# Kernel tuning notes

Measured on AMD Instinct MI355X. Metric: run time of the kernel, lower is better.

## Reference

```python
import jax, jax.numpy as jnp
import numpy as np

B, S, D_IN = 2, 2048, 2048
H, G, HD = 16, 4, 128          # num_heads, num_kv_groups, head_dim
GROUP = H // G                  # 4 query heads per kv group
D_OUT = H * HD                  # 2048
EPS = 1e-6


def _rope_tables(seq_len, head_dim, theta=10000.0):
    inv = 1.0 / (theta ** (np.arange(0, head_dim, 2, dtype=np.float32) / head_dim))
    pos = np.arange(seq_len, dtype=np.float32)
    ang = np.outer(pos, inv)                      # [S, HD/2]
    ang = np.concatenate([ang, ang], axis=-1)     # [S, HD]
    return jnp.asarray(np.cos(ang)), jnp.asarray(np.sin(ang))


def setup_inputs() -> dict:
    key = jax.random.key(0)
    ks = jax.random.split(key, 6)
    x = jax.random.normal(ks[0], (B, S, D_IN), dtype=jnp.float32)
    # Linear weights stored as [in, out] so y = x @ W (same math as nn.Linear)
    Wq = jax.random.normal(ks[1], (D_IN, 2 * D_OUT), dtype=jnp.float32) * (D_IN ** -0.5)
    Wk = jax.random.normal(ks[2], (D_IN, G * HD), dtype=jnp.float32) * (D_IN ** -0.5)
    Wv = jax.random.normal(ks[3], (D_IN, G * HD), dtype=jnp.float32) * (D_IN ** -0.5)
    Wo = jax.random.normal(ks[4], (D_OUT, D_IN), dtype=jnp.float32) * (D_OUT ** -0.5)
    q_norm_w = jnp.zeros((HD,), dtype=jnp.float32)  # Qwen-style zero-init (scale = 1 + w)
    k_norm_w = jnp.zeros((HD,), dtype=jnp.float32)
    cos, sin = _rope_tables(S, HD)
    mask = jnp.triu(jnp.ones((S, S), dtype=bool), k=1)  # causal: True above diagonal is masked
    return {"x": x, "Wq": Wq, "Wk": Wk, "Wv": Wv, "Wo": Wo,
            "q_norm_w": q_norm_w, "k_norm_w": k_norm_w,
            "cos": cos, "sin": sin, "mask": mask}


def _rmsnorm(x, w):
    xf = x.astype(jnp.float32)
    n = xf * jax.lax.rsqrt(jnp.mean(xf * xf, axis=-1, keepdims=True) + EPS)
    return (n * (1.0 + w.astype(jnp.float32))).astype(x.dtype)


def _apply_rope(x, cos, sin):
    # x: [..., S, HD]; full-dim rotation (rot_dim == head_dim)
    s = x.shape[-2]
    c = cos[:s][None, None]
    sn = sin[:s][None, None]
    x1, x2 = x[..., : HD // 2], x[..., HD // 2 :]
    rotated = jnp.concatenate([-x2, x1], axis=-1)
    return (x * c + rotated * sn).astype(x.dtype)


def reference(x, Wq, Wk, Wv, Wo, q_norm_w, k_norm_w, cos, sin, mask):
    b, s, _ = x.shape
    qg = (x @ Wq).reshape(b, s, H, 2 * HD)
    q, gate = qg[..., :HD], qg[..., HD:]
    gate = gate.reshape(b, s, D_OUT)
    q = q.transpose(0, 2, 1, 3)                                 # [b,H,s,HD]
    k = (x @ Wk).reshape(b, s, G, HD).transpose(0, 2, 1, 3)     # [b,G,s,HD]
    v = (x @ Wv).reshape(b, s, G, HD).transpose(0, 2, 1, 3)
    q = _rmsnorm(q, q_norm_w)
    k = _rmsnorm(k, k_norm_w)
    q = _apply_rope(q, cos, sin)
    k = _apply_rope(k, cos, sin)
    # GQA: group query heads by kv group instead of repeat_interleave on k/v
    qg4 = q.reshape(b, G, GROUP, s, HD)
    scores = jnp.einsum("bgjqd,bgkd->bgjqk", qg4, k)            # [b,G,GROUP,s,s]
    scores = jnp.where(mask[None, None, None], -jnp.inf, scores)
    w = jax.nn.softmax((scores * (HD ** -0.5)).astype(jnp.float32), axis=-1).astype(q.dtype)
    ctx = jnp.einsum("bgjqk,bgkd->bgjqd", w, v)                 # [b,G,GROUP,s,HD]
    ctx = ctx.reshape(b, H, s, HD).transpose(0, 2, 1, 3).reshape(b, s, D_OUT)
    ctx = ctx * jax.nn.sigmoid(gate)
    return ctx @ Wo
```

## Files before the change

### kernel.cpp

```cpp
#include <hip/hip_runtime.h>

#define S_LEN 2048
#define NROWS 4096
#define DIN   2048
#define DQKV  5120
#define DQG   4096

typedef __bf16 bf16x8 __attribute__((ext_vector_type(8)));
typedef float  floatx4 __attribute__((ext_vector_type(4)));
typedef unsigned short u16;

#define QK_SCALE 0.08838834764831845f

__device__ __forceinline__ u16 f2bf(float f) {
  unsigned int u = __float_as_uint(f);
  u += 0x7fffu + ((u >> 16) & 1u);
  return (u16)(u >> 16);
}
__device__ __forceinline__ float bf2f(u16 v) {
  return __uint_as_float(((unsigned int)v) << 16);
}
__device__ __forceinline__ int swz(int col, int row) {
  return (col & ~63) | ((((col >> 3) & 7) ^ (row & 7)) << 3) | (col & 7);
}

__device__ __forceinline__ void gload_lds16(const void* g, void* l) {
  __builtin_amdgcn_global_load_lds(
      (__attribute__((address_space(1))) void*)(void*)(g),
      (__attribute__((address_space(3))) void*)(l), 16, 0, 0);
}

__global__ __launch_bounds__(256) void cvt_x(const float* __restrict__ src,
                                             u16* __restrict__ dst) {
  const int i = blockIdx.x * 256 + threadIdx.x;
  const int row = i >> 9, col = (i & 511) << 2;
  const float4 v = reinterpret_cast<const float4*>(src)[i];
  ushort4 o;
  o.x = f2bf(v.x); o.y = f2bf(v.y); o.z = f2bf(v.z); o.w = f2bf(v.w);
  *reinterpret_cast<ushort4*>(dst + (size_t)row * DIN + swz(col, row)) = o;
}

__global__ __launch_bounds__(256) void tcvt(const float* __restrict__ src,
                                            u16* __restrict__ dst,
                                            int R, int C, int dld) {
  __shared__ float tile[32][33];
  const int c0 = blockIdx.x * 32, r0 = blockIdx.y * 32;
  const int t = threadIdx.x;
  {
    const int rl = t >> 3, cl4 = (t & 7) * 4;
    const float4 v = *reinterpret_cast<const float4*>(src + (size_t)(r0 + rl) * C + c0 + cl4);
    tile[rl][cl4 + 0] = v.x; tile[rl][cl4 + 1] = v.y;
    tile[rl][cl4 + 2] = v.z; tile[rl][cl4 + 3] = v.w;
  }
  __syncthreads();
  {
    const int cl = t >> 3, rl4 = (t & 7) * 4;
    ushort4 o;
    o.x = f2bf(tile[rl4 + 0][cl]); o.y = f2bf(tile[rl4 + 1][cl]);
    o.z = f2bf(tile[rl4 + 2][cl]); o.w = f2bf(tile[rl4 + 3][cl]);
    const int rd = c0 + cl, cd = r0 + rl4;
    *reinterpret_cast<ushort4*>(dst + (size_t)rd * dld + swz(cd, rd)) = o;
  }
}

template <bool BF16_OUT>
__global__ __launch_bounds__(256) void gemm_bt(const u16* __restrict__ A,
                                               const u16* __restrict__ Bt,
                                               void* __restrict__ Cv,
                                               int M, int N, int K) {
  __shared__ __align__(16) u16 As[128 * 64];
  __shared__ __align__(16) u16 Bs[128 * 64];
  const int tid = threadIdx.x, wv = tid >> 6, lane = tid & 63;
  const int m0 = blockIdx.y * 128, n0 = blockIdx.x * 128;
  const int wm = (wv >> 1) * 64, wn = (wv & 1) * 64;
  const int frow = lane & 15, quad = lane >> 4, fsw = frow & 7;
  const int srow = lane >> 3, scol = (lane & 7) * 8;
  floatx4 acc[4][4] = {};
  for (int k0 = 0; k0 < K; k0 += 64) {
#pragma unroll
    for (int i = 0; i < 4; ++i) {
      const int rr = (wv * 4 + i) * 8;
      gload_lds16(A  + (size_t)(m0 + rr + srow) * K + k0 + scol, &As[rr * 64]);
      gload_lds16(Bt + (size_t)(n0 + rr + srow) * K + k0 + scol, &Bs[rr * 64]);
    }
    __syncthreads();
#pragma unroll
    for (int ks = 0; ks < 2; ++ks) {
      bf16x8 af[4], bfr[4];
#pragma unroll
      for (int mi = 0; mi < 4; ++mi)
        af[mi] = *reinterpret_cast<const bf16x8*>(
            &As[(wm + mi * 16 + frow) * 64 + (((ks * 4 + quad) ^ fsw) << 3)]);
#pragma unroll
      for (int ni = 0; ni < 4; ++ni)
        bfr[ni] = *reinterpret_cast<const bf16x8*>(
            &Bs[(wn + ni * 16 + frow) * 64 + (((ks * 4 + quad) ^ fsw) << 3)]);
#pragma unroll
      for (int mi = 0; mi < 4; ++mi)
#pragma unroll
        for (int ni = 0; ni < 4; ++ni)
          acc[mi][ni] = __builtin_amdgcn_mfma_f32_16x16x32_bf16(af[mi], bfr[ni], acc[mi][ni], 0, 0, 0);
    }
    __syncthreads();
  }
  const int crow = (lane >> 4) * 4, ccol = lane & 15;
#pragma unroll
  for (int mi = 0; mi < 4; ++mi)
#pragma unroll
    for (int ni = 0; ni < 4; ++ni) {
      const size_t base = (size_t)(m0 + wm + mi * 16 + crow) * N + (n0 + wn + ni * 16 + ccol);
      if constexpr (BF16_OUT) {
        u16* C = (u16*)Cv;
#pragma unroll
        for (int r = 0; r < 4; ++r) C[base + (size_t)r * N] = f2bf(acc[mi][ni][r]);
      } else {
        float* C = (float*)Cv;
#pragma unroll
        for (int r = 0; r < 4; ++r) C[base + (size_t)r * N] = acc[mi][ni][r];
      }
    }
}

__global__ __launch_bounds__(256) void qnorm_rope(const u16* __restrict__ QKV,
                                                  const float* __restrict__ w,
                                                  const float* __restrict__ cosT,
                                                  const float* __restrict__ sinT,
                                                  u16* __restrict__ Qb) {
  const int wv = threadIdx.x >> 6, lane = threadIdx.x & 63;
  const int idx = blockIdx.x * 4 + wv;
  const int h = idx & 15, row = idx >> 4;
  const int s = row & (S_LEN - 1), b = row >> 11;
  const u16* base = QKV + (size_t)row * DQKV + h * 256;
  const float v0 = bf2f(base[lane]), v1 = bf2f(base[lane + 64]);
  float ss = v0 * v0 + v1 * v1;
#pragma unroll
  for (int m = 32; m >= 1; m >>= 1) ss += __shfl_xor(ss, m);
  const float rn = rsqrtf(ss * (1.0f / 128.0f) + 1e-6f) * QK_SCALE;
  const float n0 = v0 * rn * (1.0f + w[lane]);
  const float n1 = v1 * rn * (1.0f + w[lane + 64]);
  const float c0 = cosT[(size_t)s * 128 + lane], c1 = cosT[(size_t)s * 128 + lane + 64];
  const float sn0 = sinT[(size_t)s * 128 + lane], sn1 = sinT[(size_t)s * 128 + lane + 64];
  u16* qb = Qb + ((size_t)(b * 16 + h) * S_LEN + s) * 128;
  qb[lane]      = f2bf(n0 * c0 - n1 * sn0);
  qb[lane + 64] = f2bf(n1 * c1 + n0 * sn1);
}

__global__ __launch_bounds__(256) void knorm_rope(const u16* __restrict__ QKV,
                                                  const float* __restrict__ w,
                                                  const float* __restrict__ cosT,
                                                  const float* __restrict__ sinT,
                                                  u16* __restrict__ Kb) {
  const int wv = threadIdx.x >> 6, lane = threadIdx.x & 63;
  const int idx = blockIdx.x * 4 + wv;
  const int g = idx & 3, row = idx >> 2;
  const int s = row & (S_LEN - 1), b = row >> 11;
  const u16* base = QKV + (size_t)row * DQKV + DQG + g * 128;
  const float v0 = bf2f(base[lane]), v1 = bf2f(base[lane + 64]);
  float ss = v0 * v0 + v1 * v1;
#pragma unroll
  for (int m = 32; m >= 1; m >>= 1) ss += __shfl_xor(ss, m);
  const float rn = rsqrtf(ss * (1.0f / 128.0f) + 1e-6f);
  const float n0 = v0 * rn * (1.0f + w[lane]);
  const float n1 = v1 * rn * (1.0f + w[lane + 64]);
  const float c0 = cosT[(size_t)s * 128 + lane], c1 = cosT[(size_t)s * 128 + lane + 64];
  const float sn0 = sinT[(size_t)s * 128 + lane], sn1 = sinT[(size_t)s * 128 + lane + 64];
  u16* kb = Kb + ((size_t)(b * 4 + g) * S_LEN + s) * 128;
  const int sw = s & 7;
  const int d0 = lane, d1 = lane + 64;
  const int p0 = (((d0 >> 3) ^ sw) << 3) | (d0 & 7);
  const int p1 = (((d1 >> 3) ^ sw) << 3) | (d1 & 7);
  kb[p0] = f2bf(n0 * c0 - n1 * sn0);
  kb[p1] = f2bf(n1 * c1 + n0 * sn1);
}

__global__ __launch_bounds__(256) void vtrans(const u16* __restrict__ QKV,
                                              u16* __restrict__ Vt) {
  __shared__ u16 tile[32][40];
  const int bg = blockIdx.z;
  const int s0 = blockIdx.x * 32, d0 = blockIdx.y * 32;
  const int b = bg >> 2, g = bg & 3;
  const int t = threadIdx.x;
  {
    const int sl = t >> 3, dl4 = (t & 7) * 4;
    const ushort4 v = *reinterpret_cast<const ushort4*>(
        QKV + (size_t)(b * S_LEN + s0 + sl) * DQKV + DQG + 512 + g * 128 + d0 + dl4);
    tile[sl][dl4 + 0] = v.x; tile[sl][dl4 + 1] = v.y;
    tile[sl][dl4 + 2] = v.z; tile[sl][dl4 + 3] = v.w;
  }
  __syncthreads();
  {
    const int dl = t >> 3, sl4 = (t & 7) * 4;
    ushort4 o;
    o.x = tile[sl4 + 0][dl]; o.y = tile[sl4 + 1][dl];
    o.z = tile[sl4 + 2][dl]; o.w = tile[sl4 + 3][dl];
    const int d = d0 + dl, s = s0 + sl4;
    const size_t base = (size_t)(bg * 128 + d) * S_LEN + (s & ~63);
    const int pos = ((((s >> 3) & 7) ^ (d & 7)) << 3) | (s & 7);
    *reinterpret_cast<ushort4*>(Vt + base + pos) = o;
  }
}

__global__ __launch_bounds__(256) void attn(const u16* __restrict__ Qb,
                                            const u16* __restrict__ Kb,
                                            const u16* __restrict__ Vt,
                                            const u16* __restrict__ QKV,
                                            u16* __restrict__ ctxg) {
  __shared__ __align__(16) u16 Ks[64 * 128];
  __shared__ __align__(16) u16 Vts[128 * 64];
  __shared__ __align__(16) u16 Ps[4][16 * 68];
  const int tid = threadIdx.x, wv = tid >> 6, lane = tid & 63;
  const int ip = blockIdx.x, bh = blockIdx.y;
  const int b = bh >> 4, h = bh & 15, g = h >> 2, bg = b * 4 + g;
  const int f = lane & 15, quad = lane >> 4, fq = quad * 8;
  const int fsw = f & 7;
  const u16* Kp = Kb + (size_t)bg * S_LEN * 128;
  const u16* Vp = Vt + (size_t)bg * 128 * S_LEN;
  u16* Pw = Ps[wv];

  for (int pass = 0; pass < 2; ++pass) {
    const int qt = pass ? 31 - ip : ip;
    const u16* Qp = Qb + ((size_t)bh * S_LEN + qt * 64 + wv * 16) * 128;
    bf16x8 aq[4];
#pragma unroll
    for (int c = 0; c < 4; ++c)
      aq[c] = *reinterpret_cast<const bf16x8*>(&Qp[(size_t)f * 128 + c * 32 + fq]);

    floatx4 o[8] = {};
    float lsum[4] = {0.f, 0.f, 0.f, 0.f};
    const int nkt = qt + 1;

    for (int kt = 0; kt < nkt; ++kt) {
      const int k0 = kt * 64;
#pragma unroll
      for (int i = 0; i < 4; ++i) {
        const int j = wv * 4 + i;
        gload_lds16(Kp + (size_t)k0 * 128 + j * 512 + lane * 8, &Ks[j * 512]);
      }
#pragma unroll
      for (int i = 0; i < 4; ++i) {
        const int r0 = (wv * 4 + i) * 8;
        gload_lds16(Vp + (size_t)(r0 + (lane >> 3)) * S_LEN + k0 + (lane & 7) * 8,
                    &Vts[r0 * 64]);
      }
      __syncthreads();

      floatx4 sc[4] = {};
#pragma unroll
      for (int c = 0; c < 4; ++c) {
#pragma unroll
        for (int n = 0; n < 4; ++n) {
          bf16x8 bk = *reinterpret_cast<const bf16x8*>(
              &Ks[(n * 16 + f) * 128 + (((4 * c + quad) ^ fsw) << 3)]);
          sc[n] = __builtin_amdgcn_mfma_f32_16x16x32_bf16(aq[c], bk, sc[n], 0, 0, 0);
        }
      }

      const int qrow0 = qt * 64 + wv * 16 + quad * 4;
#pragma unroll
      for (int n = 0; n < 4; ++n) {
        const int key = k0 + n * 16 + f;
#pragma unroll
        for (int r = 0; r < 4; ++r) {
          const float p = (key <= qrow0 + r) ? __expf(sc[n][r]) : 0.f;
          lsum[r] += p;
          Pw[(quad * 4 + r) * 68 + n * 16 + f] = f2bf(p);
        }
      }

#pragma unroll
      for (int kf = 0; kf < 2; ++kf) {
        bf16x8 pf = *reinterpret_cast<const bf16x8*>(&Pw[f * 68 + kf * 32 + fq]);
#pragma unroll
        for (int dt = 0; dt < 8; ++dt) {
          bf16x8 bv = *reinterpret_cast<const bf16x8*>(
              &Vts[(dt * 16 + f) * 64 + (((4 * kf + quad) ^ fsw) << 3)]);
          o[dt] = __builtin_amdgcn_mfma_f32_16x16x32_bf16(pf, bv, o[dt], 0, 0, 0);
        }
      }
      __syncthreads();
    }

#pragma unroll
    for (int r = 0; r < 4; ++r) {
#pragma unroll
      for (int mm = 8; mm >= 1; mm >>= 1) lsum[r] += __shfl_xor(lsum[r], mm);
    }

#pragma unroll
    for (int r = 0; r < 4; ++r) {
      const int s = qt * 64 + wv * 16 + quad * 4 + r;
      const size_t grow = (size_t)b * S_LEN + s;
      const float inv = 1.0f / lsum[r];
#pragma unroll
      for (int dt = 0; dt < 8; ++dt) {
        const int d = dt * 16 + f;
        const float gate = bf2f(QKV[grow * DQKV + h * 256 + 128 + d]);
        const float val = o[dt][r] * inv * (1.0f / (1.0f + __expf(-gate)));
        const int col = h * 128 + d;
        ctxg[grow * 2048 + swz(col, (int)grow)] = f2bf(val);
      }
    }
  }
}

extern "C" void kernel_launch(void* const* d_in, const int* in_sizes, int n_in,
                              void* d_out, int out_size, void* d_ws, size_t ws_size,
                              hipStream_t stream) {
  const float* x    = (const float*)d_in[0];
  const float* Wq   = (const float*)d_in[1];
  const float* Wk   = (const float*)d_in[2];
  const float* Wv   = (const float*)d_in[3];
  const float* Wo   = (const float*)d_in[4];
  const float* qnw  = (const float*)d_in[5];
  const float* knw  = (const float*)d_in[6];
  const float* cosT = (const float*)d_in[7];
  const float* sinT = (const float*)d_in[8];

  char* p = (char*)d_ws;
  u16*   xb    = (u16*)p;  p += (size_t)NROWS * DIN * 2;
  u16*   WqkvT = (u16*)p;  p += (size_t)DQKV * DIN * 2;
  u16*   WoT   = (u16*)p;  p += (size_t)2048 * 2048 * 2;
  u16*   QKVb  = (u16*)p;  p += (size_t)NROWS * DQKV * 2;
  u16*   Qbf   = (u16*)p;  p += (size_t)2 * 16 * S_LEN * 128 * 2;
  u16*   Kbf   = (u16*)p;  p += (size_t)2 * 4 * S_LEN * 128 * 2;
  u16*   Vtb   = (u16*)p;  p += (size_t)2 * 4 * S_LEN * 128 * 2;
  u16*   ctxg  = (u16*)p;  p += (size_t)NROWS * 2048 * 2;

  cvt_x<<<8192, 256, 0, stream>>>(x, xb);
  tcvt<<<dim3(128, 64), 256, 0, stream>>>(Wq, WqkvT, 2048, 4096, 2048);
  tcvt<<<dim3(16, 64), 256, 0, stream>>>(Wk, WqkvT + (size_t)4096 * 2048, 2048, 512, 2048);
  tcvt<<<dim3(16, 64), 256, 0, stream>>>(Wv, WqkvT + (size_t)4608 * 2048, 2048, 512, 2048);
  tcvt<<<dim3(64, 64), 256, 0, stream>>>(Wo, WoT, 2048, 2048, 2048);

  gemm_bt<true><<<dim3(40, 32), 256, 0, stream>>>(xb, WqkvT, QKVb, NROWS, DQKV, DIN);

  qnorm_rope<<<16384, 256, 0, stream>>>(QKVb, qnw, cosT, sinT, Qbf);
  knorm_rope<<<4096, 256, 0, stream>>>(QKVb, knw, cosT, sinT, Kbf);
  vtrans<<<dim3(64, 4, 8), 256, 0, stream>>>(QKVb, Vtb);

  attn<<<dim3(16, 32), 256, 0, stream>>>(Qbf, Kbf, Vtb, QKVb, ctxg);

  gemm_bt<false><<<dim3(16, 32), 256, 0, stream>>>(ctxg, WoT, (float*)d_out, NROWS, 2048, 2048);
}
```

Measured before the change: 395.2 us.

## Load K and V straight from global memory in attention, dropping LDS staging

The attention kernel no longer stages K and V tiles into shared memory with swizzled async loads and barriers. Each wave now reads its MFMA operands directly from global memory, relying on the cache to absorb reuse across the four waves. The K and V producer kernels write plain unswizzled layouts to match. The paired causal q-tile scheme is replaced by one block per q-tile with a launch-bounds occupancy hint. This removes LDS traffic and syncs, but each wave repeats the same global loads, and the simple 1D grid brings back load imbalance across the causal tiles.

```diff
diff --git a/kernel.cpp b/kernel.cpp
--- a/kernel.cpp
+++ b/kernel.cpp
@@ -165,12 +165,8 @@
   const float c0 = cosT[(size_t)s * 128 + lane], c1 = cosT[(size_t)s * 128 + lane + 64];
   const float sn0 = sinT[(size_t)s * 128 + lane], sn1 = sinT[(size_t)s * 128 + lane + 64];
   u16* kb = Kb + ((size_t)(b * 4 + g) * S_LEN + s) * 128;
-  const int sw = s & 7;
-  const int d0 = lane, d1 = lane + 64;
-  const int p0 = (((d0 >> 3) ^ sw) << 3) | (d0 & 7);
-  const int p1 = (((d1 >> 3) ^ sw) << 3) | (d1 & 7);
-  kb[p0] = f2bf(n0 * c0 - n1 * sn0);
-  kb[p1] = f2bf(n1 * c1 + n0 * sn1);
+  kb[lane]      = f2bf(n0 * c0 - n1 * sn0);
+  kb[lane + 64] = f2bf(n1 * c1 + n0 * sn1);
 }
 
 __global__ __launch_bounds__(256) void vtrans(const u16* __restrict__ QKV,
@@ -193,112 +189,91 @@
     ushort4 o;
     o.x = tile[sl4 + 0][dl]; o.y = tile[sl4 + 1][dl];
     o.z = tile[sl4 + 2][dl]; o.w = tile[sl4 + 3][dl];
-    const int d = d0 + dl, s = s0 + sl4;
-    const size_t base = (size_t)(bg * 128 + d) * S_LEN + (s & ~63);
-    const int pos = ((((s >> 3) & 7) ^ (d & 7)) << 3) | (s & 7);
-    *reinterpret_cast<ushort4*>(Vt + base + pos) = o;
-  }
-}
-
-__global__ __launch_bounds__(256) void attn(const u16* __restrict__ Qb,
-                                            const u16* __restrict__ Kb,
-                                            const u16* __restrict__ Vt,
-                                            const u16* __restrict__ QKV,
-                                            u16* __restrict__ ctxg) {
-  __shared__ __align__(16) u16 Ks[64 * 128];
-  __shared__ __align__(16) u16 Vts[128 * 64];
+    *reinterpret_cast<ushort4*>(Vt + (size_t)(bg * 128 + d0 + dl) * S_LEN + s0 + sl4) = o;
+  }
+}
+
+__global__ __launch_bounds__(256, 3) void attn(const u16* __restrict__ Qb,
+                                               const u16* __restrict__ Kb,
+                                               const u16* __restrict__ Vt,
+                                               const u16* __restrict__ QKV,
+                                               u16* __restrict__ ctxg) {
   __shared__ __align__(16) u16 Ps[4][16 * 68];
   const int tid = threadIdx.x, wv = tid >> 6, lane = tid & 63;
-  const int ip = blockIdx.x, bh = blockIdx.y;
+  const int qt = blockIdx.x, bh = blockIdx.y;
   const int b = bh >> 4, h = bh & 15, g = h >> 2, bg = b * 4 + g;
   const int f = lane & 15, quad = lane >> 4, fq = quad * 8;
-  const int fsw = f & 7;
   const u16* Kp = Kb + (size_t)bg * S_LEN * 128;
   const u16* Vp = Vt + (size_t)bg * 128 * S_LEN;
   u16* Pw = Ps[wv];
 
-  for (int pass = 0; pass < 2; ++pass) {
-    const int qt = pass ? 31 - ip : ip;
-    const u16* Qp = Qb + ((size_t)bh * S_LEN + qt * 64 + wv * 16) * 128;
-    bf16x8 aq[4];
-#pragma unroll
-    for (int c = 0; c < 4; ++c)
-      aq[c] = *reinterpret_cast<const bf16x8*>(&Qp[(size_t)f * 128 + c * 32 + fq]);
-
-    floatx4 o[8] = {};
-    float lsum[4] = {0.f, 0.f, 0.f, 0.f};
-    const int nkt = qt + 1;
-
-    for (int kt = 0; kt < nkt; ++kt) {
-      const int k0 = kt * 64;
-#pragma unroll
-      for (int i = 0; i < 4; ++i) {
-        const int j = wv * 4 + i;
-        gload_lds16(Kp + (size_t)k0 * 128 + j * 512 + lane * 8, &Ks[j * 512]);
+  const u16* Qp = Qb + ((size_t)bh * S_LEN + qt * 64 + wv * 16) * 128;
+  bf16x8 aq[4];
+#pragma unroll
+  for (int c = 0; c < 4; ++c)
+    aq[c] = *reinterpret_cast<const bf16x8*>(&Qp[(size_t)f * 128 + c * 32 + fq]);
+
+  floatx4 o[8] = {};
+  float lsum[4] = {0.f, 0.f, 0.f, 0.f};
+  const int nkt = qt + 1;
+
+  for (int kt = 0; kt < nkt; ++kt) {
+    const int k0 = kt * 64;
+    floatx4 sc[4] = {};
+#pragma unroll
+    for (int c = 0; c < 4; ++c) {
+      bf16x8 bk[4];
+#pragma unroll
+      for (int n = 0; n < 4; ++n)
+        bk[n] = *reinterpret_cast<const bf16x8*>(
+            &Kp[(size_t)(k0 + n * 16 + f) * 128 + c * 32 + fq]);
+#pragma unroll
+      for (int n = 0; n < 4; ++n)
+        sc[n] = __builtin_amdgcn_mfma_f32_16x16x32_bf16(aq[c], bk[n], sc[n], 0, 0, 0);
+    }
+
+    const int qrow0 = qt * 64 + wv * 16 + quad * 4;
+#pragma unroll
+    for (int n = 0; n < 4; ++n) {
+      const int key = k0 + n * 16 + f;
+#pragma unroll
+      for (int r = 0; r < 4; ++r) {
+        const float p = (key <= qrow0 + r) ? __expf(sc[n][r]) : 0.f;
+        lsum[r] += p;
+        Pw[(quad * 4 + r) * 68 + n * 16 + f] = f2bf(p);
       }
-#pragma unroll
-      for (int i = 0; i < 4; ++i) {
-        const int r0 = (wv * 4 + i) * 8;
-        gload_lds16(Vp + (size_t)(r0 + (lane >> 3)) * S_LEN + k0 + (lane & 7) * 8,
-                    &Vts[r0 * 64]);
+    }
+
+#pragma unroll
+    for (int kf = 0; kf < 2; ++kf) {
+      bf16x8 pf = *reinterpret_cast<const bf16x8*>(&Pw[f * 68 + kf * 32 + fq]);
+#pragma unroll
+      for (int dt = 0; dt < 8; ++dt) {
+        bf16x8 bv = *reinterpret_cast<const bf16x8*>(
+            &Vp[(size_t)(dt * 16 + f) * S_LEN + k0 + kf * 32 + fq]);
+        o[dt] = __builtin_amdgcn_mfma_f32_16x16x32_bf16(pf, bv, o[dt], 0, 0, 0);
       }
-      __syncthreads();
-
-      floatx4 sc[4] = {};
-#pragma unroll
-      for (int c = 0; c < 4; ++c) {
-#pragma unroll
-        for (int n = 0; n < 4; ++n) {
-          bf16x8 bk = *reinterpret_cast<const bf16x8*>(
-              &Ks[(n * 16 + f) * 128 + (((4 * c + quad) ^ fsw) << 3)]);
-          sc[n] = __builtin_amdgcn_mfma_f32_16x16x32_bf16(aq[c], bk, sc[n], 0, 0, 0);
-        }
-      }
-
-      const int qrow0 = qt * 64 + wv * 16 + quad * 4;
-#pragma unroll
-      for (int n = 0; n < 4; ++n) {
-        const int key = k0 + n * 16 + f;
-#pragma unroll
-        for (int r = 0; r < 4; ++r) {
-          const float p = (key <= qrow0 + r) ? __expf(sc[n][r]) : 0.f;
-          lsum[r] += p;
-          Pw[(quad * 4 + r) * 68 + n * 16 + f] = f2bf(p);
-        }
-      }
-
-#pragma unroll
-      for (int kf = 0; kf < 2; ++kf) {
-        bf16x8 pf = *reinterpret_cast<const bf16x8*>(&Pw[f * 68 + kf * 32 + fq]);
-#pragma unroll
-        for (int dt = 0; dt < 8; ++dt) {
-          bf16x8 bv = *reinterpret_cast<const bf16x8*>(
-              &Vts[(dt * 16 + f) * 64 + (((4 * kf + quad) ^ fsw) << 3)]);
-          o[dt] = __builtin_amdgcn_mfma_f32_16x16x32_bf16(pf, bv, o[dt], 0, 0, 0);
-        }
-      }
-      __syncthreads();
-    }
-
-#pragma unroll
-    for (int r = 0; r < 4; ++r) {
-#pragma unroll
-      for (int mm = 8; mm >= 1; mm >>= 1) lsum[r] += __shfl_xor(lsum[r], mm);
-    }
-
-#pragma unroll
-    for (int r = 0; r < 4; ++r) {
-      const int s = qt * 64 + wv * 16 + quad * 4 + r;
-      const size_t grow = (size_t)b * S_LEN + s;
-      const float inv = 1.0f / lsum[r];
-#pragma unroll
-      for (int dt = 0; dt < 8; ++dt) {
-        const int d = dt * 16 + f;
-        const float gate = bf2f(QKV[grow * DQKV + h * 256 + 128 + d]);
-        const float val = o[dt][r] * inv * (1.0f / (1.0f + __expf(-gate)));
-        const int col = h * 128 + d;
-        ctxg[grow * 2048 + swz(col, (int)grow)] = f2bf(val);
-      }
+    }
+  }
+
+#pragma unroll
+  for (int r = 0; r < 4; ++r) {
+#pragma unroll
+    for (int mm = 8; mm >= 1; mm >>= 1) lsum[r] += __shfl_xor(lsum[r], mm);
+  }
+
+#pragma unroll
+  for (int r = 0; r < 4; ++r) {
+    const int s = qt * 64 + wv * 16 + quad * 4 + r;
+    const size_t grow = (size_t)b * S_LEN + s;
+    const float inv = 1.0f / lsum[r];
+#pragma unroll
+    for (int dt = 0; dt < 8; ++dt) {
+      const int d = dt * 16 + f;
+      const float gate = bf2f(QKV[grow * DQKV + h * 256 + 128 + d]);
+      const float val = o[dt][r] * inv * (1.0f / (1.0f + __expf(-gate)));
+      const int col = h * 128 + d;
+      ctxg[grow * 2048 + swz(col, (int)grow)] = f2bf(val);
     }
   }
 }
@@ -338,7 +313,7 @@
   knorm_rope<<<4096, 256, 0, stream>>>(QKVb, knw, cosT, sinT, Kbf);
   vtrans<<<dim3(64, 4, 8), 256, 0, stream>>>(QKVb, Vtb);
 
-  attn<<<dim3(16, 32), 256, 0, stream>>>(Qbf, Kbf, Vtb, QKVb, ctxg);
+  attn<<<dim3(32, 32), 256, 0, stream>>>(Qbf, Kbf, Vtb, QKVb, ctxg);
 
   gemm_bt<false><<<dim3(16, 32), 256, 0, stream>>>(ctxg, WoT, (float*)d_out, NROWS, 2048, 2048);
 }
```

Result: slower. 759.4 us (+92.1%).
